# Performance work log

Hardware: AMD Instinct MI355X
Metric: run time of the kernel (lower is better)

The kernel has to match this reference:

```python
import jax, jax.numpy as jnp
import numpy as np

N, E, G = 20000, 320000, 64
IN_DIM, HID, HEADS, NCLS = 512, 256, 2, 10
EPS = 1e-5
SLOPE = 0.2


def setup_inputs() -> dict:
    key = jax.random.key(0)
    ks = jax.random.split(key, 24)
    s = 0.02
    inp = {
        "feat": jax.random.normal(ks[0], (N, IN_DIM), jnp.float32),
        "src": jax.random.randint(ks[1], (E,), 0, N, jnp.int32),
        "dst": jax.random.randint(ks[2], (E,), 0, N, jnp.int32),
        "graph_ids": jnp.sort(jax.random.randint(ks[3], (N,), 0, G, jnp.int32)),
        # GATv2Conv params (fc_src, fc_dst, attn)
        "W_src": jax.random.normal(ks[4], (IN_DIM, HEADS * HID), jnp.float32) * s,
        "b_src": jnp.zeros((HEADS * HID,), jnp.float32),
        "W_dst": jax.random.normal(ks[5], (IN_DIM, HEADS * HID), jnp.float32) * s,
        "b_dst": jnp.zeros((HEADS * HID,), jnp.float32),
        "attn": jax.random.normal(ks[6], (HEADS, HID), jnp.float32) * s,
        # skip_lin: input_dim -> 2*hidden
        "W_skip": jax.random.normal(ks[7], (IN_DIM, 2 * HID), jnp.float32) * s,
        "b_skip": jnp.zeros((2 * HID,), jnp.float32),
        # bn1 affine
        "gamma": jnp.ones((2 * HID,), jnp.float32),
        "beta": jnp.zeros((2 * HID,), jnp.float32),
        # dim_reducer
        "W_red": jax.random.normal(ks[8], (2 * HID, HID), jnp.float32) * s,
        "b_red": jnp.zeros((HID,), jnp.float32),
        # attention-pool gate Linear(hidden, 1)
        "w_gate": jax.random.normal(ks[9], (HID, 1), jnp.float32) * s,
        "b_gate": jnp.zeros((1,), jnp.float32),
        # classifier MLP
        "W1": jax.random.normal(ks[10], (HID, HID // 2), jnp.float32) * s,
        "b1": jnp.zeros((HID // 2,), jnp.float32),
        "W2": jax.random.normal(ks[11], (HID // 2, NCLS), jnp.float32) * s,
        "b2": jnp.zeros((NCLS,), jnp.float32),
    }
    return inp


def _gatv2(feat, src, dst, W_src, b_src, W_dst, b_dst, attn):
    # feat_src/feat_dst: [N, H, D]
    fs = (feat @ W_src + b_src).reshape(N, HEADS, HID)
    fd = (feat @ W_dst + b_dst).reshape(N, HEADS, HID)
    fs_e = fs[src]                               # [E, H, D]
    m = jax.nn.leaky_relu(fs_e + fd[dst], SLOPE)  # [E, H, D]
    e = jnp.einsum("ehd,hd->eh", m, attn)         # [E, H]
    # edge softmax grouped by destination node
    e_max = jax.ops.segment_max(e, dst, num_segments=N)          # [N, H]
    e_exp = jnp.exp(e - e_max[dst])                               # [E, H]
    denom = jax.ops.segment_sum(e_exp, dst, num_segments=N)      # [N, H]
    alpha = e_exp / denom[dst]                                    # [E, H]
    out = jax.ops.segment_sum(alpha[:, :, None] * fs_e, dst, num_segments=N)
    return out  # [N, H, D]; zero rows for zero in-degree nodes


def reference(feat, src, dst, graph_ids, W_src, b_src, W_dst, b_dst, attn,
              W_skip, b_skip, gamma, beta, W_red, b_red, w_gate, b_gate,
              W1, b1, W2, b2):
    h1 = jax.nn.elu(_gatv2(feat, src, dst, W_src, b_src, W_dst, b_dst, attn))
    h1 = h1.reshape(N, HEADS * HID)
    h1 = h1 + (feat @ W_skip + b_skip)
    # BatchNorm1d (training-mode batch statistics, biased variance)
    mu = jnp.mean(h1, axis=0)
    var = jnp.mean((h1 - mu) ** 2, axis=0)
    h1 = (h1 - mu) * jax.lax.rsqrt(var + EPS) * gamma + beta
    hr = h1 @ W_red + b_red                      # [N, HID]
    # GlobalAttentionPooling: segment softmax of gate scores over each graph
    gate = hr @ w_gate + b_gate                  # [N, 1]
    g_max = jax.ops.segment_max(gate, graph_ids, num_segments=G)
    g_exp = jnp.exp(gate - g_max[graph_ids])
    g_den = jax.ops.segment_sum(g_exp, graph_ids, num_segments=G)
    a = g_exp / g_den[graph_ids]                 # [N, 1]
    h_g = jax.ops.segment_sum(a * hr, graph_ids, num_segments=G)  # [G, HID]
    # classifier (dropout = identity at inference)
    return jax.nn.relu(h_g @ W1 + b1) @ W2 + b2  # [G, NCLS]
```

## Files before the change

kernel.cpp:

```cpp
#include <hip/hip_runtime.h>
#include <math.h>

#define N_NODES 20000
#define N_EDGES 320000
#define N_GRAPH 64
#define IN_DIM  512
#define HID     256
#define F2      512
#define EPS_BN  1e-5f
#define SLOPE   0.2f
#define SCAN_BLOCKS 79

typedef unsigned short u16;
typedef __attribute__((ext_vector_type(8))) short bf16x8;
typedef __attribute__((ext_vector_type(4))) float floatx4;

__device__ __forceinline__ u16 bf_hi(float x) {
    unsigned int u = __float_as_uint(x);
    return (u16)((u + 0x7fffu + ((u >> 16) & 1u)) >> 16);
}
__device__ __forceinline__ float bf_val(u16 h) {
    return __uint_as_float((unsigned int)h << 16);
}
__device__ __forceinline__ void unpack2(unsigned int u, float& lo, float& hi) {
    lo = __uint_as_float(u << 16);
    hi = __uint_as_float(u & 0xffff0000u);
}
__device__ __forceinline__ float lr(float x) { return fmaxf(x, SLOPE * x); }

__global__ void init_zero_kernel(int* counts, int* cursor, float* stats,
                                 float* h_gnum, float* gden) {
    int i = blockIdx.x * blockDim.x + threadIdx.x;
    if (i < N_NODES) { counts[i] = 0; cursor[i] = 0; }
    if (i < 1024) stats[i] = 0.f;
    if (i < N_GRAPH * HID) h_gnum[i] = 0.f;
    if (i < N_GRAPH) gden[i] = 0.f;
}

__global__ __launch_bounds__(256) void split_feat_kernel(
    const float* __restrict__ X, u16* __restrict__ Hi, int total8) {
    int i = blockIdx.x * 256 + threadIdx.x;
    if (i >= total8) return;
    size_t base = (size_t)i * 8;
    float4 x0 = *(const float4*)(X + base);
    float4 x1 = *(const float4*)(X + base + 4);
    float xs[8] = {x0.x, x0.y, x0.z, x0.w, x1.x, x1.y, x1.z, x1.w};
    union { u16 s[8]; uint4 v; } h;
#pragma unroll
    for (int j = 0; j < 8; j++) h.s[j] = bf_hi(xs[j]);
    *(uint4*)(Hi + base) = h.v;
}

__global__ __launch_bounds__(256) void split_wt_kernel(
    const float* __restrict__ Ws, const float* __restrict__ Wd,
    const float* __restrict__ Wk, const float* __restrict__ Wr,
    u16* __restrict__ Hi, u16* __restrict__ Lo) {
    __shared__ float t[32][33];
    int w = blockIdx.z;
    int ncols = (w == 3) ? 256 : 512;
    int n0 = blockIdx.y * 32;
    if (n0 >= ncols) return;
    const float* W = (w == 0) ? Ws : ((w == 1) ? Wd : ((w == 2) ? Wk : Wr));
    size_t obase = (size_t)w * 512 * 512;
    int k0 = blockIdx.x * 32;
    int tx = threadIdx.x, ty = threadIdx.y;
#pragma unroll
    for (int i = 0; i < 4; i++)
        t[ty * 4 + i][tx] = W[(size_t)(k0 + ty * 4 + i) * ncols + n0 + tx];
    __syncthreads();
#pragma unroll
    for (int i = 0; i < 4; i++) {
        float x = t[tx][ty * 4 + i];
        u16 hh = bf_hi(x);
        size_t o = obase + (size_t)(n0 + ty * 4 + i) * 512 + k0 + tx;
        Hi[o] = hh;
        Lo[o] = bf_hi(x - bf_val(hh));
    }
}

__global__ __launch_bounds__(256) void gemm_mfma_triple(
    const u16* __restrict__ Fhi, const u16* __restrict__ Wthi,
    const float* __restrict__ b_src, const float* __restrict__ b_dst,
    const float* __restrict__ b_skip,
    u16* __restrict__ FS16, u16* __restrict__ FD16, float* __restrict__ h1) {
    __shared__ u16 AsHi[128 * 40];
    int tid = threadIdx.x;
    int w_idx = blockIdx.y >> 2;
    int col0 = (blockIdx.y & 3) * 128;
    int row0 = blockIdx.x * 128;
    int lane = tid & 63, wave = tid >> 6;
    int wm = (wave & 1) * 64, wn = (wave >> 1) * 64;
    int quad = lane >> 4, l16 = lane & 15;

    int sr = tid >> 1, sh = (tid & 1) * 16;
    int grow = row0 + sr;
    bool ok = grow < N_NODES;
    u16* sA = &AsHi[sr * 40 + sh];
    const u16* Wb = Wthi + (size_t)w_idx * 512 * 512;

    floatx4 acc[4][4];
#pragma unroll
    for (int i = 0; i < 4; i++)
#pragma unroll
        for (int j = 0; j < 4; j++) acc[i][j] = (floatx4){0.f, 0.f, 0.f, 0.f};

    for (int k0 = 0; k0 < 512; k0 += 32) {
        uint4 a0 = make_uint4(0, 0, 0, 0), a1 = a0;
        if (ok) {
            const u16* g = Fhi + (size_t)grow * 512 + k0 + sh;
            a0 = *(const uint4*)(g);
            a1 = *(const uint4*)(g + 8);
        }
        union { uint4 u; bf16x8 v; } bh[4];
#pragma unroll
        for (int nt = 0; nt < 4; nt++) {
            size_t off = (size_t)(col0 + wn + nt * 16 + l16) * 512 + k0 + quad * 8;
            bh[nt].u = *(const uint4*)(Wb + off);
        }
        __syncthreads();
        *(uint4*)(sA + 0) = a0;
        *(uint4*)(sA + 8) = a1;
        __syncthreads();
#pragma unroll
        for (int mt = 0; mt < 4; mt++) {
            int me = (wm + mt * 16 + l16) * 40 + quad * 8;
            bf16x8 ah = *(const bf16x8*)&AsHi[me];
#pragma unroll
            for (int nt = 0; nt < 4; nt++)
                acc[mt][nt] = __builtin_amdgcn_mfma_f32_16x16x32_bf16(ah, bh[nt].v, acc[mt][nt], 0, 0, 0);
        }
    }

    const float* bias = (w_idx == 0) ? b_src : ((w_idx == 1) ? b_dst : b_skip);
    float bv[4];
#pragma unroll
    for (int nt = 0; nt < 4; nt++) bv[nt] = bias[col0 + wn + nt * 16 + l16];
#pragma unroll
    for (int mt = 0; mt < 4; mt++) {
#pragma unroll
        for (int r = 0; r < 4; r++) {
            int m = row0 + wm + mt * 16 + quad * 4 + r;
            if (m < N_NODES) {
#pragma unroll
                for (int nt = 0; nt < 4; nt++) {
                    int n = col0 + wn + nt * 16 + l16;
                    float vv = acc[mt][nt][r] + bv[nt];
                    if (w_idx == 0)      FS16[(size_t)m * 512 + n] = bf_hi(vv);
                    else if (w_idx == 1) FD16[(size_t)m * 512 + n] = bf_hi(vv);
                    else                 h1[(size_t)m * 512 + n] = vv;
                }
            }
        }
    }
}

__global__ __launch_bounds__(256) void gemm_mfma_red(
    const float* __restrict__ Af,
    const u16* __restrict__ Bhi, const u16* __restrict__ Blo,
    const float* __restrict__ bias, float* __restrict__ C,
    int Nrows, int M,
    const float* __restrict__ bscale, const float* __restrict__ bshift) {
    __shared__ u16 AsHi[128 * 40];
    __shared__ u16 AsLo[128 * 40];
    __shared__ float sBN[1024];
    int tid = threadIdx.x;
    int row0 = blockIdx.x * 128;
    int col0 = blockIdx.y * 128;
    int lane = tid & 63, wave = tid >> 6;
    int wm = (wave & 1) * 64, wn = (wave >> 1) * 64;
    int quad = lane >> 4, l16 = lane & 15;

    sBN[tid] = bscale[tid]; sBN[256 + tid] = bscale[256 + tid];
    sBN[512 + tid] = bshift[tid]; sBN[768 + tid] = bshift[256 + tid];
    __syncthreads();

    int sr = tid >> 1, sh = (tid & 1) * 16;
    int grow = row0 + sr;
    bool ok = grow < Nrows;
    u16* sA_hi = &AsHi[sr * 40 + sh];
    u16* sA_lo = &AsLo[sr * 40 + sh];

    floatx4 acc[4][4];
#pragma unroll
    for (int i = 0; i < 4; i++)
#pragma unroll
        for (int j = 0; j < 4; j++) acc[i][j] = (floatx4){0.f, 0.f, 0.f, 0.f};

    for (int k0 = 0; k0 < 512; k0 += 32) {
        float v[16];
        if (ok) {
            const float* g = Af + (size_t)grow * 512 + k0 + sh;
            *(float4*)&v[0]  = *(const float4*)(g);
            *(float4*)&v[4]  = *(const float4*)(g + 4);
            *(float4*)&v[8]  = *(const float4*)(g + 8);
            *(float4*)&v[12] = *(const float4*)(g + 12);
        } else {
#pragma unroll
            for (int j = 0; j < 16; j++) v[j] = 0.f;
        }
        union { u16 s[8]; uint4 u; } h0_, h1_, l0_, l1_;
#pragma unroll
        for (int j = 0; j < 16; j++) {
            int kc = k0 + sh + j;
            float x = v[j] * sBN[kc] + sBN[512 + kc];
            u16 hh = bf_hi(x);
            u16 ll = bf_hi(x - bf_val(hh));
            if (j < 8) { h0_.s[j] = hh; l0_.s[j] = ll; }
            else       { h1_.s[j - 8] = hh; l1_.s[j - 8] = ll; }
        }
        union { uint4 u; bf16x8 v; } bh[4], bl[4];
#pragma unroll
        for (int nt = 0; nt < 4; nt++) {
            size_t off = (size_t)(col0 + wn + nt * 16 + l16) * 512 + k0 + quad * 8;
            bh[nt].u = *(const uint4*)(Bhi + off);
            bl[nt].u = *(const uint4*)(Blo + off);
        }
        __syncthreads();
        *(uint4*)(sA_hi + 0) = h0_.u;
        *(uint4*)(sA_hi + 8) = h1_.u;
        *(uint4*)(sA_lo + 0) = l0_.u;
        *(uint4*)(sA_lo + 8) = l1_.u;
        __syncthreads();
#pragma unroll
        for (int mt = 0; mt < 4; mt++) {
            int me = (wm + mt * 16 + l16) * 40 + quad * 8;
            bf16x8 ah = *(const bf16x8*)&AsHi[me];
            bf16x8 al = *(const bf16x8*)&AsLo[me];
#pragma unroll
            for (int nt = 0; nt < 4; nt++) {
                acc[mt][nt] = __builtin_amdgcn_mfma_f32_16x16x32_bf16(ah, bh[nt].v, acc[mt][nt], 0, 0, 0);
                acc[mt][nt] = __builtin_amdgcn_mfma_f32_16x16x32_bf16(ah, bl[nt].v, acc[mt][nt], 0, 0, 0);
                acc[mt][nt] = __builtin_amdgcn_mfma_f32_16x16x32_bf16(al, bh[nt].v, acc[mt][nt], 0, 0, 0);
            }
        }
    }

    float bv[4];
#pragma unroll
    for (int nt = 0; nt < 4; nt++) bv[nt] = bias[col0 + wn + nt * 16 + l16];
#pragma unroll
    for (int mt = 0; mt < 4; mt++) {
#pragma unroll
        for (int r = 0; r < 4; r++) {
            int m = row0 + wm + mt * 16 + quad * 4 + r;
            if (m < Nrows) {
#pragma unroll
                for (int nt = 0; nt < 4; nt++) {
                    int n = col0 + wn + nt * 16 + l16;
                    C[(size_t)m * M + n] = acc[mt][nt][r] + bv[nt];
                }
            }
        }
    }
}

__global__ void hist_kernel(const int* __restrict__ dst, int* __restrict__ counts) {
    int e = blockIdx.x * blockDim.x + threadIdx.x;
    if (e < N_EDGES) atomicAdd(&counts[dst[e]], 1);
}

__global__ __launch_bounds__(256) void scan_local_kernel(
    const int* __restrict__ counts, int* __restrict__ row_ptr, int* __restrict__ bsum) {
    __shared__ int buf[256];
    int b = blockIdx.x, tid = threadIdx.x;
    int i = b * 256 + tid;
    buf[tid] = (i < N_NODES) ? counts[i] : 0;
    __syncthreads();
    for (int off = 1; off < 256; off <<= 1) {
        int t = (tid >= off) ? buf[tid - off] : 0;
        __syncthreads();
        buf[tid] += t;
        __syncthreads();
    }
    if (i < N_NODES) row_ptr[i + 1] = buf[tid];
    if (tid == 255) bsum[b] = buf[255];
}

__global__ __launch_bounds__(256) void scan_fixup_kernel(
    const int* __restrict__ bsum, int* __restrict__ row_ptr) {
    __shared__ int red[256];
    int b = blockIdx.x, tid = threadIdx.x;
    red[tid] = (tid < b) ? bsum[tid] : 0;
    __syncthreads();
    for (int off = 128; off > 0; off >>= 1) {
        if (tid < off) red[tid] += red[tid + off];
        __syncthreads();
    }
    int offset = red[0];
    int i = b * 256 + tid;
    if (i < N_NODES) row_ptr[i + 1] += offset;
    if (b == 0 && tid == 0) row_ptr[0] = 0;
}

__global__ void scatter_kernel(const int* __restrict__ src, const int* __restrict__ dst,
                               const int* __restrict__ row_ptr,
                               int* __restrict__ cursor, int* __restrict__ csr_src) {
    int e = blockIdx.x * blockDim.x + threadIdx.x;
    if (e < N_EDGES) {
        int d = dst[e];
        int pos = atomicAdd(&cursor[d], 1);
        csr_src[row_ptr[d] + pos] = src[e];
    }
}

__global__ __launch_bounds__(256) void edge_fused_kernel(
    const u16* __restrict__ FS16, const u16* __restrict__ FD16,
    const float* __restrict__ attn, const int* __restrict__ csr_src,
    const int* __restrict__ row_ptr, float* __restrict__ h1) {
    __shared__ float red[3 * 512];
    __shared__ float den[2];
    int n = blockIdx.x, tid = threadIdx.x;
    int lane = tid & 63, wave = tid >> 6;
    int beg = row_ptr[n], end = row_ptr[n + 1], deg = end - beg;
    if (tid < 2) den[tid] = 0.f;

    float fdv[8], aw[8];
    {
        uint4 q = *(const uint4*)(FD16 + (size_t)n * 512 + 8 * lane);
        unpack2(q.x, fdv[0], fdv[1]); unpack2(q.y, fdv[2], fdv[3]);
        unpack2(q.z, fdv[4], fdv[5]); unpack2(q.w, fdv[6], fdv[7]);
        float4 a0 = *(const float4*)(attn + 8 * lane);
        float4 a1 = *(const float4*)(attn + 8 * lane + 4);
        aw[0] = a0.x; aw[1] = a0.y; aw[2] = a0.z; aw[3] = a0.w;
        aw[4] = a1.x; aw[5] = a1.y; aw[6] = a1.z; aw[7] = a1.w;
    }
    __syncthreads();

    float acc[8] = {0.f, 0.f, 0.f, 0.f, 0.f, 0.f, 0.f, 0.f};
    float dp = 0.f;
    for (int j = wave; j < deg; j += 4) {
        int s = csr_src[beg + j];
        uint4 q = *(const uint4*)(FS16 + (size_t)s * 512 + 8 * lane);
        float f[8];
        unpack2(q.x, f[0], f[1]); unpack2(q.y, f[2], f[3]);
        unpack2(q.z, f[4], f[5]); unpack2(q.w, f[6], f[7]);
        float p = 0.f;
#pragma unroll
        for (int k = 0; k < 8; k++) p += lr(f[k] + fdv[k]) * aw[k];
#pragma unroll
        for (int off = 16; off > 0; off >>= 1) p += __shfl_xor(p, off, 64);
        float ex = expf(p);
#pragma unroll
        for (int k = 0; k < 8; k++) acc[k] += ex * f[k];
        if ((lane & 31) == 0) dp += ex;
    }
    if ((lane & 31) == 0) atomicAdd(&den[lane >> 5], dp);

    if (wave > 0) {
        float* r = &red[(wave - 1) * 512 + lane * 8];
        *(float4*)(r + 0) = *(float4*)&acc[0];
        *(float4*)(r + 4) = *(float4*)&acc[4];
    }
    __syncthreads();
    if (wave == 0) {
#pragma unroll
        for (int w = 0; w < 3; w++) {
            const float* r = &red[w * 512 + lane * 8];
#pragma unroll
            for (int k = 0; k < 8; k++) acc[k] += r[k];
        }
        float d = (lane < 32) ? den[0] : den[1];
        float inv = d > 0.f ? 1.f / d : 0.f;
        float* hp = h1 + (size_t)n * 512 + 8 * lane;
        float4 s0 = *(float4*)(hp);
        float4 s1 = *(float4*)(hp + 4);
        float v[8];
#pragma unroll
        for (int k = 0; k < 8; k++) {
            float x = acc[k] * inv;
            v[k] = x > 0.f ? x : expm1f(x);
        }
        s0.x += v[0]; s0.y += v[1]; s0.z += v[2]; s0.w += v[3];
        s1.x += v[4]; s1.y += v[5]; s1.z += v[6]; s1.w += v[7];
        *(float4*)(hp) = s0;
        *(float4*)(hp + 4) = s1;
    }
}

__global__ __launch_bounds__(256) void bn_stats_kernel(const float* __restrict__ h1,
                                                       float* __restrict__ stats,
                                                       int rows_per_block) {
    int tid = threadIdx.x;
    int r0 = blockIdx.x * rows_per_block;
    int r1 = min(r0 + rows_per_block, N_NODES);
    float s0 = 0.f, q0 = 0.f, s1 = 0.f, q1 = 0.f;
    for (int r = r0; r < r1; r++) {
        float a = h1[(size_t)r * F2 + tid];
        float b = h1[(size_t)r * F2 + 256 + tid];
        s0 += a; q0 += a * a;
        s1 += b; q1 += b * b;
    }
    atomicAdd(&stats[tid], s0);
    atomicAdd(&stats[256 + tid], s1);
    atomicAdd(&stats[512 + tid], q0);
    atomicAdd(&stats[512 + 256 + tid], q1);
}

__global__ void bn_finalize_kernel(const float* __restrict__ stats,
                                   const float* __restrict__ gamma,
                                   const float* __restrict__ beta,
                                   float* __restrict__ bscale, float* __restrict__ bshift) {
    int c = threadIdx.x;
    float mu = stats[c] / (float)N_NODES;
    float var = stats[512 + c] / (float)N_NODES - mu * mu;
    float sc = gamma[c] * rsqrtf(var + EPS_BN);
    bscale[c] = sc;
    bshift[c] = beta[c] - mu * sc;
}

__global__ __launch_bounds__(256) void gate_kernel(const float* __restrict__ hr,
                                                   const float* __restrict__ wg,
                                                   float* __restrict__ gate) {
    int n = blockIdx.x * 4 + (threadIdx.x >> 6);
    int lane = threadIdx.x & 63;
    const float4* row = (const float4*)(hr + (size_t)n * HID);
    const float4* w = (const float4*)wg;
    float4 a = row[lane], b = w[lane];
    float p = a.x * b.x + a.y * b.y + a.z * b.z + a.w * b.w;
#pragma unroll
    for (int off = 32; off > 0; off >>= 1) p += __shfl_down(p, off, 64);
    if (lane == 0) gate[n] = p;
}

__device__ __forceinline__ int lower_bound_dev(const int* a, int n, int v) {
    int lo = 0, hi = n;
    while (lo < hi) {
        int mid = (lo + hi) >> 1;
        if (a[mid] < v) lo = mid + 1; else hi = mid;
    }
    return lo;
}

__global__ __launch_bounds__(256) void pool_partial_kernel(
    const float* __restrict__ hr, const float* __restrict__ gate,
    const int* __restrict__ gids, float* __restrict__ h_gnum,
    float* __restrict__ gden) {
    int b = blockIdx.x;
    int g = b >> 3, part = b & 7;
    int tid = threadIdx.x;
    int start = lower_bound_dev(gids, N_NODES, g);
    int end = lower_bound_dev(gids, N_NODES, g + 1);
    int span = end - start;
    int p_beg = start + (span * part) / 8;
    int p_end = start + (span * (part + 1)) / 8;
    if (p_beg >= p_end) return;
    __shared__ float wa[256];
    __shared__ float red[256];
    float acc = 0.f, denacc = 0.f;
    for (int cbeg = p_beg; cbeg < p_end; cbeg += 256) {
        int c = min(256, p_end - cbeg);
        float e = 0.f;
        if (tid < c) { e = expf(gate[cbeg + tid]); wa[tid] = e; }
        red[tid] = (tid < c) ? e : 0.f;
        __syncthreads();
        for (int off = 128; off > 0; off >>= 1) {
            if (tid < off) red[tid] += red[tid + off];
            __syncthreads();
        }
        denacc += red[0];
        for (int i = 0; i < c; i++) acc += wa[i] * hr[(size_t)(cbeg + i) * HID + tid];
        __syncthreads();
    }
    atomicAdd(&h_gnum[g * HID + tid], acc);
    if (tid == 0) atomicAdd(&gden[g], denacc);
}

__global__ __launch_bounds__(128) void classifier_kernel(
    const float* __restrict__ h_gnum, const float* __restrict__ gden,
    const float* __restrict__ W1, const float* __restrict__ b1,
    const float* __restrict__ W2, const float* __restrict__ b2,
    float* __restrict__ out) {
    int g = blockIdx.x;
    int tid = threadIdx.x;
    __shared__ float hg[256];
    __shared__ float z1[128];
    float d = gden[g];
    float invd = d > 0.f ? 1.f / d : 0.f;
    hg[tid] = h_gnum[g * HID + tid] * invd;
    hg[tid + 128] = h_gnum[g * HID + tid + 128] * invd;
    __syncthreads();
    float a = b1[tid];
#pragma unroll 8
    for (int k = 0; k < 256; k++) a += hg[k] * W1[k * 128 + tid];
    z1[tid] = a > 0.f ? a : 0.f;
    __syncthreads();
    if (tid < 10) {
        float o = b2[tid];
#pragma unroll 8
        for (int j = 0; j < 128; j++) o += z1[j] * W2[j * 10 + tid];
        out[g * 10 + tid] = o;
    }
}

extern "C" void kernel_launch(void* const* d_in, const int* in_sizes, int n_in,
                              void* d_out, int out_size, void* d_ws, size_t ws_size,
                              hipStream_t stream) {
    const float* feat   = (const float*)d_in[0];
    const int*   src    = (const int*)d_in[1];
    const int*   dst    = (const int*)d_in[2];
    const int*   gids   = (const int*)d_in[3];
    const float* W_src  = (const float*)d_in[4];
    const float* b_src  = (const float*)d_in[5];
    const float* W_dst  = (const float*)d_in[6];
    const float* b_dst  = (const float*)d_in[7];
    const float* attn   = (const float*)d_in[8];
    const float* W_skip = (const float*)d_in[9];
    const float* b_skip = (const float*)d_in[10];
    const float* gamma  = (const float*)d_in[11];
    const float* beta   = (const float*)d_in[12];
    const float* W_red  = (const float*)d_in[13];
    const float* b_red  = (const float*)d_in[14];
    const float* w_gate = (const float*)d_in[15];
    const float* W1     = (const float*)d_in[17];
    const float* b1     = (const float*)d_in[18];
    const float* W2     = (const float*)d_in[19];
    const float* b2     = (const float*)d_in[20];
    float* out = (float*)d_out;

    char* p = (char*)d_ws;
    auto alloc = [&](size_t bytes) -> char* {
        char* r = p;
        p += (bytes + 255) & ~(size_t)255;
        return r;
    };
    u16*   FS16     = (u16*)alloc((size_t)N_NODES * F2 * 2);
    u16*   FD16     = (u16*)alloc((size_t)N_NODES * F2 * 2);
    float* h1       = (float*)alloc((size_t)N_NODES * F2 * 4);
    float* gate     = (float*)alloc((size_t)N_NODES * 4);
    float* stats    = (float*)alloc(1024 * 4);
    float* bn_scale = (float*)alloc(512 * 4);
    float* bn_shift = (float*)alloc(512 * 4);
    float* h_gnum   = (float*)alloc((size_t)N_GRAPH * HID * 4);
    float* gden     = (float*)alloc((size_t)N_GRAPH * 4);
    int* counts     = (int*)alloc((size_t)N_NODES * 4);
    int* row_ptr    = (int*)alloc((size_t)(N_NODES + 1) * 4);
    int* cursor     = (int*)alloc((size_t)N_NODES * 4);
    int* csr_src    = (int*)alloc((size_t)N_EDGES * 4);
    int* bsum       = (int*)alloc((size_t)SCAN_BLOCKS * 4);
    u16* Fhi        = (u16*)alloc((size_t)N_NODES * IN_DIM * 2);
    u16* Wthi       = (u16*)alloc((size_t)4 * 512 * 512 * 2);
    u16* Wtlo       = (u16*)alloc((size_t)4 * 512 * 512 * 2);
    float* hr = (float*)Fhi;
    (void)ws_size; (void)in_sizes; (void)n_in; (void)out_size;

    const size_t WSZ = (size_t)512 * 512;

    init_zero_kernel<<<(N_NODES + 255) / 256, 256, 0, stream>>>(counts, cursor, stats, h_gnum, gden);
    split_feat_kernel<<<(N_NODES * IN_DIM / 8 + 255) / 256, 256, 0, stream>>>(
        feat, Fhi, N_NODES * IN_DIM / 8);
    split_wt_kernel<<<dim3(16, 16, 4), dim3(32, 8), 0, stream>>>(
        W_src, W_dst, W_skip, W_red, Wthi, Wtlo);

    gemm_mfma_triple<<<dim3((N_NODES + 127) / 128, 12), 256, 0, stream>>>(
        Fhi, Wthi, b_src, b_dst, b_skip, FS16, FD16, h1);

    hist_kernel<<<(N_EDGES + 255) / 256, 256, 0, stream>>>(dst, counts);
    scan_local_kernel<<<SCAN_BLOCKS, 256, 0, stream>>>(counts, row_ptr, bsum);
    scan_fixup_kernel<<<SCAN_BLOCKS, 256, 0, stream>>>(bsum, row_ptr);
    scatter_kernel<<<(N_EDGES + 255) / 256, 256, 0, stream>>>(src, dst, row_ptr, cursor, csr_src);

    edge_fused_kernel<<<N_NODES, 256, 0, stream>>>(FS16, FD16, attn, csr_src, row_ptr, h1);

    bn_stats_kernel<<<500, 256, 0, stream>>>(h1, stats, 40);
    bn_finalize_kernel<<<1, 512, 0, stream>>>(stats, gamma, beta, bn_scale, bn_shift);

    dim3 g256((N_NODES + 127) / 128, 2);
    gemm_mfma_red<<<g256, 256, 0, stream>>>(
        h1, Wthi + 3 * WSZ, Wtlo + 3 * WSZ, b_red, hr, N_NODES, HID,
        bn_scale, bn_shift);

    gate_kernel<<<N_NODES / 4, 256, 0, stream>>>(hr, w_gate, gate);

    pool_partial_kernel<<<N_GRAPH * 8, 256, 0, stream>>>(hr, gate, gids, h_gnum, gden);

    classifier_kernel<<<N_GRAPH, 128, 0, stream>>>(h_gnum, gden, W1, b1, W2, b2, out);
}
```

Measured before the change: 425.8 us.

## Load GEMM A operands directly from global and remap blocks per XCD

The triple GEMM no longer stages A tiles through shared memory with two barriers per k-step. Each wave now loads its A fragments straight from global memory, and the feature buffer is zero-padded to a multiple of 128 rows so no bounds check is needed. Block indices are remapped to a 1D grid so that all 12 column/weight tiles of one row tile land on the same XCD, which should improve L2 reuse of the A rows. The cost is redundant global A loads across waves that share rows, plus a larger padded buffer and extra zero-writes in the split kernel.

```diff
diff --git a/kernel.cpp b/kernel.cpp
--- a/kernel.cpp
+++ b/kernel.cpp
@@ -10,6 +10,8 @@
 #define EPS_BN  1e-5f
 #define SLOPE   0.2f
 #define SCAN_BLOCKS 79
+#define N_RT    157
+#define RT_PAD  20096
 
 typedef unsigned short u16;
 typedef __attribute__((ext_vector_type(8))) short bf16x8;
@@ -38,10 +40,14 @@
 }
 
 __global__ __launch_bounds__(256) void split_feat_kernel(
-    const float* __restrict__ X, u16* __restrict__ Hi, int total8) {
+    const float* __restrict__ X, u16* __restrict__ Hi, int total8, int pad8) {
     int i = blockIdx.x * 256 + threadIdx.x;
-    if (i >= total8) return;
+    if (i >= pad8) return;
     size_t base = (size_t)i * 8;
+    if (i >= total8) {
+        *(uint4*)(Hi + base) = make_uint4(0, 0, 0, 0);
+        return;
+    }
     float4 x0 = *(const float4*)(X + base);
     float4 x1 = *(const float4*)(X + base + 4);
     float xs[8] = {x0.x, x0.y, x0.z, x0.w, x1.x, x1.y, x1.z, x1.w};
@@ -83,20 +89,28 @@
     const float* __restrict__ b_src, const float* __restrict__ b_dst,
     const float* __restrict__ b_skip,
     u16* __restrict__ FS16, u16* __restrict__ FD16, float* __restrict__ h1) {
-    __shared__ u16 AsHi[128 * 40];
+    int b = blockIdx.x;
+    int xcd = b & 7, slot = b >> 3;
+    int rt = (slot / 12) * 8 + xcd;
+    if (rt >= N_RT) return;
+    int cw = slot % 12;
+    int w_idx = cw >> 2;
+    int col0 = (cw & 3) * 128;
+    int row0 = rt * 128;
     int tid = threadIdx.x;
-    int w_idx = blockIdx.y >> 2;
-    int col0 = (blockIdx.y & 3) * 128;
-    int row0 = blockIdx.x * 128;
     int lane = tid & 63, wave = tid >> 6;
     int wm = (wave & 1) * 64, wn = (wave >> 1) * 64;
     int quad = lane >> 4, l16 = lane & 15;
 
-    int sr = tid >> 1, sh = (tid & 1) * 16;
-    int grow = row0 + sr;
-    bool ok = grow < N_NODES;
-    u16* sA = &AsHi[sr * 40 + sh];
     const u16* Wb = Wthi + (size_t)w_idx * 512 * 512;
+    const u16* aP[4];
+    const u16* bP[4];
+#pragma unroll
+    for (int mt = 0; mt < 4; mt++)
+        aP[mt] = Fhi + (size_t)(row0 + wm + mt * 16 + l16) * 512 + quad * 8;
+#pragma unroll
+    for (int nt = 0; nt < 4; nt++)
+        bP[nt] = Wb + (size_t)(col0 + wn + nt * 16 + l16) * 512 + quad * 8;
 
     floatx4 acc[4][4];
 #pragma unroll
@@ -104,31 +118,18 @@
 #pragma unroll
         for (int j = 0; j < 4; j++) acc[i][j] = (floatx4){0.f, 0.f, 0.f, 0.f};
 
+#pragma unroll 2
     for (int k0 = 0; k0 < 512; k0 += 32) {
-        uint4 a0 = make_uint4(0, 0, 0, 0), a1 = a0;
-        if (ok) {
-            const u16* g = Fhi + (size_t)grow * 512 + k0 + sh;
-            a0 = *(const uint4*)(g);
-            a1 = *(const uint4*)(g + 8);
-        }
-        union { uint4 u; bf16x8 v; } bh[4];
-#pragma unroll
-        for (int nt = 0; nt < 4; nt++) {
-            size_t off = (size_t)(col0 + wn + nt * 16 + l16) * 512 + k0 + quad * 8;
-            bh[nt].u = *(const uint4*)(Wb + off);
-        }
-        __syncthreads();
-        *(uint4*)(sA + 0) = a0;
-        *(uint4*)(sA + 8) = a1;
-        __syncthreads();
-#pragma unroll
-        for (int mt = 0; mt < 4; mt++) {
-            int me = (wm + mt * 16 + l16) * 40 + quad * 8;
-            bf16x8 ah = *(const bf16x8*)&AsHi[me];
+        union { uint4 u; bf16x8 v; } a[4], bb[4];
+#pragma unroll
+        for (int mt = 0; mt < 4; mt++) a[mt].u = *(const uint4*)(aP[mt] + k0);
+#pragma unroll
+        for (int nt = 0; nt < 4; nt++) bb[nt].u = *(const uint4*)(bP[nt] + k0);
+#pragma unroll
+        for (int mt = 0; mt < 4; mt++)
 #pragma unroll
             for (int nt = 0; nt < 4; nt++)
-                acc[mt][nt] = __builtin_amdgcn_mfma_f32_16x16x32_bf16(ah, bh[nt].v, acc[mt][nt], 0, 0, 0);
-        }
+                acc[mt][nt] = __builtin_amdgcn_mfma_f32_16x16x32_bf16(a[mt].v, bb[nt].v, acc[mt][nt], 0, 0, 0);
     }
 
     const float* bias = (w_idx == 0) ? b_src : ((w_idx == 1) ? b_dst : b_skip);
@@ -537,7 +538,7 @@
     int* cursor     = (int*)alloc((size_t)N_NODES * 4);
     int* csr_src    = (int*)alloc((size_t)N_EDGES * 4);
     int* bsum       = (int*)alloc((size_t)SCAN_BLOCKS * 4);
-    u16* Fhi        = (u16*)alloc((size_t)N_NODES * IN_DIM * 2);
+    u16* Fhi        = (u16*)alloc((size_t)RT_PAD * IN_DIM * 2);
     u16* Wthi       = (u16*)alloc((size_t)4 * 512 * 512 * 2);
     u16* Wtlo       = (u16*)alloc((size_t)4 * 512 * 512 * 2);
     float* hr = (float*)Fhi;
@@ -546,12 +547,12 @@
     const size_t WSZ = (size_t)512 * 512;
 
     init_zero_kernel<<<(N_NODES + 255) / 256, 256, 0, stream>>>(counts, cursor, stats, h_gnum, gden);
-    split_feat_kernel<<<(N_NODES * IN_DIM / 8 + 255) / 256, 256, 0, stream>>>(
-        feat, Fhi, N_NODES * IN_DIM / 8);
+    split_feat_kernel<<<(RT_PAD * IN_DIM / 8 + 255) / 256, 256, 0, stream>>>(
+        feat, Fhi, N_NODES * IN_DIM / 8, RT_PAD * IN_DIM / 8);
     split_wt_kernel<<<dim3(16, 16, 4), dim3(32, 8), 0, stream>>>(
         W_src, W_dst, W_skip, W_red, Wthi, Wtlo);
 
-    gemm_mfma_triple<<<dim3((N_NODES + 127) / 128, 12), 256, 0, stream>>>(
+    gemm_mfma_triple<<<dim3(((N_RT + 7) / 8) * 8 * 12), 256, 0, stream>>>(
         Fhi, Wthi, b_src, b_dst, b_skip, FS16, FD16, h1);
 
     hist_kernel<<<(N_EDGES + 255) / 256, 256, 0, stream>>>(dst, counts);
```

Result: slower. 477.7 us (+12.2%).
